# Kernel optimization log

Hardware: AMD Instinct MI355X
Metric: run time of the kernel (lower is better)

## Reference

```python
import jax, jax.numpy as jnp
import numpy as np

N_KERNELS = 5
MUL_FACTOR = 2.0


def setup_inputs() -> dict:
    key = jax.random.key(0)
    k1, k2 = jax.random.split(key)
    X = jax.random.normal(k1, (4096, 512), dtype=jnp.float32)
    Y = jax.random.normal(k2, (4096, 512), dtype=jnp.float32)
    return {"X": X, "Y": Y}


def _mmd(X, Y):
    # multipliers: 2.0 ** (arange(5) - 2) = [0.25, 0.5, 1, 2, 4]
    mults = MUL_FACTOR ** (jnp.arange(N_KERNELS, dtype=jnp.float32) - N_KERNELS // 2)
    Z = jnp.concatenate([X, Y], axis=0)            # [N+M, D]
    n = Z.shape[0]
    # squared euclidean pairwise distances (cdist ** 2)
    sq = jnp.sum(Z * Z, axis=-1)                    # [N+M]
    D2 = sq[:, None] + sq[None, :] - 2.0 * (Z @ Z.T)
    D2 = jnp.maximum(D2, 0.0)                       # [N+M, N+M]
    # bandwidth from detached distances: sum / (n^2 - n)
    bw = jax.lax.stop_gradient(jnp.sum(D2)) / (n * n - n)
    # multi-bandwidth RBF sum over kernels
    K = jnp.sum(jnp.exp(-D2[None, :, :] / (bw * mults)[:, None, None]), axis=0)
    Nx = X.shape[0]
    XX = jnp.mean(K[:Nx, :Nx])
    XY = jnp.mean(K[:Nx, Nx:])
    YY = jnp.mean(K[Nx:, Nx:])
    return XX - 2.0 * XY + YY


def reference(X, Y):
    return _mmd(X, Y)
```

## Files before the change

kernel.cpp:

```cpp
#include <hip/hip_runtime.h>

#define N_ROWS 8192
#define NX     4096
#define DIM    512
#define BT     128
#define NT     64
#define NTRI   2080
#define BK     32

typedef __bf16 bf16_t;
typedef bf16_t bf16x8 __attribute__((ext_vector_type(8)));
typedef float  f32x4  __attribute__((ext_vector_type(4)));

#if __has_builtin(__builtin_amdgcn_exp2f)
  #define EXP2F __builtin_amdgcn_exp2f
#else
  #define EXP2F exp2f
#endif


__device__ __forceinline__ const float* zrow(const float* X, const float* Y, int r) {
    return (r < NX) ? (X + (size_t)r * DIM) : (Y + (size_t)(r - NX) * DIM);
}

__device__ __forceinline__ void gload_lds16(const bf16_t* g, bf16_t* l) {
    __builtin_amdgcn_global_load_lds(
        (__attribute__((address_space(1))) void*)(void*)(g),
        (__attribute__((address_space(3))) void*)(void*)(l), 16, 0, 0);
}

__global__ void k_prep(const float* __restrict__ X, const float* __restrict__ Y,
                       bf16_t* __restrict__ Zh, float* __restrict__ sqrow,
                       float* __restrict__ colsum, unsigned* __restrict__ tk1,
                       double* __restrict__ S1acc) {
    int t = threadIdx.x;
    if (blockIdx.x == 0) {
        colsum[t] = 0.f; colsum[t + 256] = 0.f;
        if (t == 0) { *tk1 = 0u; *S1acc = 0.0; }
    }
    int wv = t >> 6, lane = t & 63;
    int row = blockIdx.x * 4 + wv;
    const float4* z4 = (const float4*)zrow(X, Y, row);
    float4 a = z4[lane * 2], b = z4[lane * 2 + 1];
    bf16x8 h;
    h[0] = (bf16_t)a.x; h[1] = (bf16_t)a.y; h[2] = (bf16_t)a.z; h[3] = (bf16_t)a.w;
    h[4] = (bf16_t)b.x; h[5] = (bf16_t)b.y; h[6] = (bf16_t)b.z; h[7] = (bf16_t)b.w;
    *(bf16x8*)(Zh + (size_t)row * DIM + lane * 8) = h;
    float s = a.x*a.x + a.y*a.y + a.z*a.z + a.w*a.w
            + b.x*b.x + b.y*b.y + b.z*b.z + b.w*b.w;
    #pragma unroll
    for (int off = 32; off > 0; off >>= 1) s += __shfl_down(s, off);
    if (lane == 0) sqrow[row] = s;
}

__global__ __launch_bounds__(512) void k_colsum(const bf16_t* __restrict__ Zh,
                                                const float* __restrict__ sqrow,
                                                float* __restrict__ colsum,
                                                float* __restrict__ cvals,
                                                double* __restrict__ S1acc,
                                                unsigned* __restrict__ tk1,
                                                double* __restrict__ acc,
                                                unsigned* __restrict__ tk2) {
    __shared__ float red[8][4][8];
    __shared__ double dred[512];
    __shared__ int is_last;
    int t = threadIdx.x, lane = t & 63, wv = t >> 6;
    int n16 = lane & 15, q16 = lane >> 4;
    int g = blockIdx.x & 15, slab = blockIdx.x >> 4;
    int c0 = g * 32 + q16 * 8;
    float s[8] = {0.f, 0.f, 0.f, 0.f, 0.f, 0.f, 0.f, 0.f};
    #pragma unroll
    for (int it = 0; it < 8; ++it) {
        int r = slab * 1024 + it * 128 + wv * 16 + n16;
        bf16x8 v = *(const bf16x8*)(Zh + (size_t)r * DIM + c0);
        #pragma unroll
        for (int j = 0; j < 8; ++j) s[j] += (float)v[j];
    }
    #pragma unroll
    for (int off = 8; off >= 1; off >>= 1)
        #pragma unroll
        for (int j = 0; j < 8; ++j) s[j] += __shfl_down(s[j], off);
    if (n16 == 0)
        #pragma unroll
        for (int j = 0; j < 8; ++j) red[wv][q16][j] = s[j];
    __syncthreads();
    float oldc = 0.f;
    if (t < 32) {
        int q = t >> 3, j = t & 7;
        float v = 0.f;
        #pragma unroll
        for (int w = 0; w < 8; ++w) v += red[w][q][j];
        oldc = atomicAdd(&colsum[g * 32 + q * 8 + j], v);
    }
    double olds = 0.0;
    if (g == 0) {
        int i = slab * 1024 + t;
        double d = (double)sqrow[i] + (double)sqrow[i + 512];
        #pragma unroll
        for (int off = 32; off > 0; off >>= 1) d += __shfl_down(d, off);
        if (lane == 0) olds = atomicAdd(S1acc, d);
    }
    asm volatile("" :: "v"(oldc), "v"(olds));
    asm volatile("s_waitcnt vmcnt(0)" ::: "memory");
    __syncthreads();
    if (t == 0) is_last = (atomicAdd(tk1, 1u) == 127u);
    __syncthreads();
    if (!is_last) return;
    float cv = atomicAdd(&colsum[t], 0.f);
    dred[t] = (double)cv * (double)cv;
    __syncthreads();
    for (int off = 256; off > 0; off >>= 1) {
        if (t < off) dred[t] += dred[t + off];
        __syncthreads();
    }
    if (t < 8) acc[t * 16] = 0.0;
    if (t == 0) {
        double S1 = atomicAdd(S1acc, 0.0);
        double n = (double)N_ROWS;
        double sumD2 = 2.0 * n * S1 - 2.0 * dred[0];
        double bw = sumD2 / (n * n - n);
        const double LOG2E = 1.4426950408889634;
        double mult = 0.25;
        for (int k = 0; k < 5; ++k) {
            cvals[k] = (float)(-LOG2E / (bw * mult));
            mult *= 2.0;
        }
        *tk2 = 0u;
    }
}

__global__ __launch_bounds__(256, 3) void k_pair(const bf16_t* __restrict__ Zh,
                                                 const float* __restrict__ sqrow,
                                                 const float* __restrict__ cvals,
                                                 double* __restrict__ acc,
                                                 unsigned* __restrict__ tk2,
                                                 float* __restrict__ out) {
    int L0 = blockIdx.x;
    int q = (L0 & 7) * (NTRI / 8) + (L0 >> 3);
    int ti, tj;
    {
        int I = 0, rem = q;
        #pragma unroll
        for (int it = 0; it < 8; ++it) {
            int rowcnt = 36 + (7 - I) * 64;
            if (rem >= rowcnt && I < 7) { rem -= rowcnt; ++I; } else break;
        }
        if (rem < 36) {
            int a = 0;
            #pragma unroll
            for (int it = 0; it < 7; ++it) {
                int nxt = (a + 1) * 8 - (a + 1) * a / 2;
                if (nxt <= rem) ++a; else break;
            }
            int off = a * 8 - a * (a - 1) / 2;
            ti = I * 8 + a;
            tj = I * 8 + a + (rem - off);
        } else {
            int r2 = rem - 36;
            int J = I + 1 + (r2 >> 6);
            int w = r2 & 63;
            ti = I * 8 + (w >> 3);
            tj = J * 8 + (w & 7);
        }
    }

    __shared__ bf16_t As[3][4096];
    __shared__ bf16_t Bs[3][4096];
    __shared__ float wsum[4];

    int t = threadIdx.x, lane = t & 63, wv = t >> 6;
    int wr = wv >> 1, wc = wv & 1;
    int i0 = ti * BT + wr * 64;
    int j0 = tj * BT + wc * 64;

    const bf16_t* gA[2]; const bf16_t* gB[2];
    {
        int c0 = t, r0 = c0 >> 2, sq0 = c0 & 3, q0 = sq0 ^ ((r0 >> 1) & 3);
        int c1 = 256 + t, r1 = c1 >> 2, sq1 = c1 & 3, q1 = sq1 ^ ((r1 >> 1) & 3);
        gA[0] = Zh + (size_t)(ti * BT + r0) * DIM + q0 * 8;
        gB[0] = Zh + (size_t)(tj * BT + r0) * DIM + q0 * 8;
        gA[1] = Zh + (size_t)(ti * BT + r1) * DIM + q1 * 8;
        gB[1] = Zh + (size_t)(tj * BT + r1) * DIM + q1 * 8;
    }
    int ldsoff0 = (wv * 64) * 8;
    int ldsoff1 = (256 + wv * 64) * 8;

    int n16 = lane & 15, q16 = lane >> 4;
    int aoff[4], boff[4];
    #pragma unroll
    for (int aa = 0; aa < 4; ++aa) {
        int r = 16 * (wr * 4 + aa) + n16;
        aoff[aa] = (r * 4 + (q16 ^ ((r >> 1) & 3))) * 8;
    }
    #pragma unroll
    for (int bb = 0; bb < 4; ++bb) {
        int r = 16 * (wc * 4 + bb) + n16;
        boff[bb] = (r * 4 + (q16 ^ ((r >> 1) & 3))) * 8;
    }

    float c4 = cvals[4];
    float sqi[4][4], sqj[4];
    #pragma unroll
    for (int aa = 0; aa < 4; ++aa)
        #pragma unroll
        for (int r = 0; r < 4; ++r)
            sqi[aa][r] = sqrow[i0 + 16 * aa + q16 * 4 + r];
    #pragma unroll
    for (int bb = 0; bb < 4; ++bb)
        sqj[bb] = sqrow[j0 + 16 * bb + n16];

    f32x4 accf[4][4];
    #pragma unroll
    for (int a = 0; a < 4; ++a)
        #pragma unroll
        for (int b = 0; b < 4; ++b)
            accf[a][b] = (f32x4){0.f, 0.f, 0.f, 0.f};

#define STAGE(S) do {                                   \
        int _b = (S) % 3; int _kn = (S) * BK;           \
        gload_lds16(gA[0] + _kn, &As[_b][ldsoff0]);     \
        gload_lds16(gB[0] + _kn, &Bs[_b][ldsoff0]);     \
        gload_lds16(gA[1] + _kn, &As[_b][ldsoff1]);     \
        gload_lds16(gB[1] + _kn, &Bs[_b][ldsoff1]);     \
    } while (0)

#define KSTEP(S, VM, DO_STAGE) do {                                          \
        asm volatile("s_waitcnt vmcnt(" VM ")" ::: "memory");                \
        __builtin_amdgcn_s_barrier();                                        \
        __builtin_amdgcn_sched_barrier(0);                                   \
        if (DO_STAGE) STAGE((S) + 2);                                        \
        const bf16_t* Ab = &As[(S) % 3][0];                                  \
        const bf16_t* Bb = &Bs[(S) % 3][0];                                  \
        bf16x8 a[4], b[4];                                                   \
        _Pragma("unroll")                                                    \
        for (int aa = 0; aa < 4; ++aa) a[aa] = *(const bf16x8*)(Ab + aoff[aa]); \
        _Pragma("unroll")                                                    \
        for (int bb = 0; bb < 4; ++bb) b[bb] = *(const bf16x8*)(Bb + boff[bb]); \
        __builtin_amdgcn_s_setprio(1);                                       \
        _Pragma("unroll")                                                    \
        for (int aa = 0; aa < 4; ++aa)                                       \
            _Pragma("unroll")                                                \
            for (int bb = 0; bb < 4; ++bb)                                   \
                accf[aa][bb] = __builtin_amdgcn_mfma_f32_16x16x32_bf16(      \
                    a[aa], b[bb], accf[aa][bb], 0, 0, 0);                    \
        __builtin_amdgcn_s_setprio(0);                                       \
    } while (0)

    STAGE(0); STAGE(1);
    KSTEP( 0, "4", 1); KSTEP( 1, "4", 1); KSTEP( 2, "4", 1); KSTEP( 3, "4", 1);
    KSTEP( 4, "4", 1); KSTEP( 5, "4", 1); KSTEP( 6, "4", 1); KSTEP( 7, "4", 1);
    KSTEP( 8, "4", 1); KSTEP( 9, "4", 1); KSTEP(10, "4", 1); KSTEP(11, "4", 1);
    KSTEP(12, "4", 1); KSTEP(13, "4", 1);
    KSTEP(14, "4", 0);
    KSTEP(15, "0", 0);
#undef KSTEP
#undef STAGE

    float s_local = 0.f;
    #pragma unroll
    for (int aa = 0; aa < 4; ++aa) {
        #pragma unroll
        for (int bb = 0; bb < 4; ++bb) {
            #pragma unroll
            for (int r = 0; r < 4; ++r) {
                float d2 = fmaf(-2.f, accf[aa][bb][r], sqi[aa][r] + sqj[bb]);
                d2 = fmaxf(d2, 0.f);
                float e4 = EXP2F(d2 * c4);
                float e3 = e4 * e4;
                float e2 = e3 * e3;
                float e1 = e2 * e2;
                float e0 = e1 * e1;
                s_local += e4 + e3 + e2 + e1 + e0;
            }
        }
    }
    #pragma unroll
    for (int off = 32; off > 0; off >>= 1) s_local += __shfl_down(s_local, off);
    if (lane == 0) wsum[wv] = s_local;
    __syncthreads();
    if (t == 0) {
        float bs = wsum[0] + wsum[1] + wsum[2] + wsum[3];
        double si = (ti < NT / 2) ? 1.0 : -1.0;
        double sj = (tj < NT / 2) ? 1.0 : -1.0;
        double w = si * sj * ((ti == tj) ? 1.0 : 2.0);
        double oldv = atomicAdd(&acc[(L0 & 7) * 16], w * (double)bs);
        asm volatile("" :: "v"(oldv));
        asm volatile("s_waitcnt vmcnt(0)" ::: "memory");
        unsigned old = atomicAdd(tk2, 1u);
        if (old == NTRI - 1) {
            double ssum = 0.0;
            #pragma unroll
            for (int i = 0; i < 8; ++i) ssum += atomicAdd(&acc[i * 16], 0.0);
            out[0] = (float)(ssum / ((double)NX * (double)NX));
        }
    }
}

extern "C" void kernel_launch(void* const* d_in, const int* in_sizes, int n_in,
                              void* d_out, int out_size, void* d_ws, size_t ws_size,
                              hipStream_t stream) {
    const float* X = (const float*)d_in[0];
    const float* Y = (const float*)d_in[1];
    float* out = (float*)d_out;

    float*    sqrow  = (float*)d_ws;
    float*    colsum = sqrow + 8192;
    float*    cvals  = (float*)((char*)d_ws + 34816);
    unsigned* tk1    = (unsigned*)((char*)d_ws + 34840);
    unsigned* tk2    = (unsigned*)((char*)d_ws + 34844);
    double*   S1acc  = (double*)((char*)d_ws + 34848);
    double*   acc    = (double*)((char*)d_ws + 34944);
    bf16_t*   Zh     = (bf16_t*)((char*)d_ws + 36864);

    k_prep  <<<2048, 256, 0, stream>>>(X, Y, Zh, sqrow, colsum, tk1, S1acc);
    k_colsum<<<128, 512, 0, stream>>>(Zh, sqrow, colsum, cvals, S1acc, tk1, acc, tk2);
    k_pair  <<<NTRI, 256, 0, stream>>>(Zh, sqrow, cvals, acc, tk2, out);
}
```

Before: 130.5 us.

## Make pair kernel persistent with cross-tile prefetch of next tile's stages

Launches 768 persistent blocks that each process two or three upper-triangle tile pairs instead of one block per tile. The first two K-stages of the next tile are prefetched during the last MFMA steps of the current tile, so the pipeline stays full across tiles. This targets block launch overhead, prologue latency and the tail of 2080 blocks spread over the CUs. It adds per-tile barriers, an atomic per tile, and a static split where some blocks get three tiles and others two, which can leave the load uneven.

```diff
diff --git a/kernel.cpp b/kernel.cpp
--- a/kernel.cpp
+++ b/kernel.cpp
@@ -7,6 +7,7 @@
 #define NT     64
 #define NTRI   2080
 #define BK     32
+#define NPERS  768
 
 typedef __bf16 bf16_t;
 typedef bf16_t bf16x8 __attribute__((ext_vector_type(8)));
@@ -135,33 +136,40 @@
                                                  double* __restrict__ acc,
                                                  unsigned* __restrict__ tk2,
                                                  float* __restrict__ out) {
-    int L0 = blockIdx.x;
-    int q = (L0 & 7) * (NTRI / 8) + (L0 >> 3);
-    int ti, tj;
-    {
-        int I = 0, rem = q;
-        #pragma unroll
-        for (int it = 0; it < 8; ++it) {
-            int rowcnt = 36 + (7 - I) * 64;
-            if (rem >= rowcnt && I < 7) { rem -= rowcnt; ++I; } else break;
-        }
-        if (rem < 36) {
-            int a = 0;
-            #pragma unroll
-            for (int it = 0; it < 7; ++it) {
-                int nxt = (a + 1) * 8 - (a + 1) * a / 2;
-                if (nxt <= rem) ++a; else break;
+    int b = blockIdx.x;
+    int ntile = (b < NTRI - 2 * NPERS) ? 3 : 2;
+    int tis[3], tjs[3];
+    #pragma unroll
+    for (int g = 0; g < 3; ++g) {
+        int T = b + g * NPERS;
+        int ti_ = 0, tj_ = 0;
+        if (T < NTRI) {
+            int q = (T & 7) * (NTRI / 8) + (T >> 3);
+            int I = 0, rem = q;
+            #pragma unroll
+            for (int it = 0; it < 8; ++it) {
+                int rowcnt = 36 + (7 - I) * 64;
+                if (rem >= rowcnt && I < 7) { rem -= rowcnt; ++I; } else break;
             }
-            int off = a * 8 - a * (a - 1) / 2;
-            ti = I * 8 + a;
-            tj = I * 8 + a + (rem - off);
-        } else {
-            int r2 = rem - 36;
-            int J = I + 1 + (r2 >> 6);
-            int w = r2 & 63;
-            ti = I * 8 + (w >> 3);
-            tj = J * 8 + (w & 7);
-        }
+            if (rem < 36) {
+                int a = 0;
+                #pragma unroll
+                for (int it = 0; it < 7; ++it) {
+                    int nxt = (a + 1) * 8 - (a + 1) * a / 2;
+                    if (nxt <= rem) ++a; else break;
+                }
+                int off = a * 8 - a * (a - 1) / 2;
+                ti_ = I * 8 + a;
+                tj_ = I * 8 + a + (rem - off);
+            } else {
+                int r2 = rem - 36;
+                int J = I + 1 + (r2 >> 6);
+                int w = r2 & 63;
+                ti_ = I * 8 + (w >> 3);
+                tj_ = J * 8 + (w & 7);
+            }
+        }
+        tis[g] = ti_; tjs[g] = tj_;
     }
 
     __shared__ bf16_t As[3][4096];
@@ -170,22 +178,14 @@
 
     int t = threadIdx.x, lane = t & 63, wv = t >> 6;
     int wr = wv >> 1, wc = wv & 1;
-    int i0 = ti * BT + wr * 64;
-    int j0 = tj * BT + wc * 64;
-
-    const bf16_t* gA[2]; const bf16_t* gB[2];
-    {
-        int c0 = t, r0 = c0 >> 2, sq0 = c0 & 3, q0 = sq0 ^ ((r0 >> 1) & 3);
-        int c1 = 256 + t, r1 = c1 >> 2, sq1 = c1 & 3, q1 = sq1 ^ ((r1 >> 1) & 3);
-        gA[0] = Zh + (size_t)(ti * BT + r0) * DIM + q0 * 8;
-        gB[0] = Zh + (size_t)(tj * BT + r0) * DIM + q0 * 8;
-        gA[1] = Zh + (size_t)(ti * BT + r1) * DIM + q1 * 8;
-        gB[1] = Zh + (size_t)(tj * BT + r1) * DIM + q1 * 8;
-    }
+    int n16 = lane & 15, q16 = lane >> 4;
+
+    int r0_, q0_, r1_, q1_;
+    { int c0 = t;       r0_ = c0 >> 2; q0_ = (c0 & 3) ^ ((r0_ >> 1) & 3);
+      int c1 = 256 + t; r1_ = c1 >> 2; q1_ = (c1 & 3) ^ ((r1_ >> 1) & 3); }
     int ldsoff0 = (wv * 64) * 8;
     int ldsoff1 = (256 + wv * 64) * 8;
 
-    int n16 = lane & 15, q16 = lane >> 4;
     int aoff[4], boff[4];
     #pragma unroll
     for (int aa = 0; aa < 4; ++aa) {
@@ -199,101 +199,145 @@
     }
 
     float c4 = cvals[4];
-    float sqi[4][4], sqj[4];
-    #pragma unroll
-    for (int aa = 0; aa < 4; ++aa)
-        #pragma unroll
-        for (int r = 0; r < 4; ++r)
-            sqi[aa][r] = sqrow[i0 + 16 * aa + q16 * 4 + r];
-    #pragma unroll
-    for (int bb = 0; bb < 4; ++bb)
-        sqj[bb] = sqrow[j0 + 16 * bb + n16];
-
-    f32x4 accf[4][4];
-    #pragma unroll
-    for (int a = 0; a < 4; ++a)
-        #pragma unroll
-        for (int b = 0; b < 4; ++b)
-            accf[a][b] = (f32x4){0.f, 0.f, 0.f, 0.f};
-
-#define STAGE(S) do {                                   \
-        int _b = (S) % 3; int _kn = (S) * BK;           \
-        gload_lds16(gA[0] + _kn, &As[_b][ldsoff0]);     \
-        gload_lds16(gB[0] + _kn, &Bs[_b][ldsoff0]);     \
-        gload_lds16(gA[1] + _kn, &As[_b][ldsoff1]);     \
-        gload_lds16(gB[1] + _kn, &Bs[_b][ldsoff1]);     \
+
+#define SETPTRS(TI, TJ, A0, B0, A1, B1) do {                        \
+        (A0) = Zh + (size_t)((TI) * BT + r0_) * DIM + q0_ * 8;      \
+        (B0) = Zh + (size_t)((TJ) * BT + r0_) * DIM + q0_ * 8;      \
+        (A1) = Zh + (size_t)((TI) * BT + r1_) * DIM + q1_ * 8;      \
+        (B1) = Zh + (size_t)((TJ) * BT + r1_) * DIM + q1_ * 8;      \
     } while (0)
 
-#define KSTEP(S, VM, DO_STAGE) do {                                          \
-        asm volatile("s_waitcnt vmcnt(" VM ")" ::: "memory");                \
-        __builtin_amdgcn_s_barrier();                                        \
-        __builtin_amdgcn_sched_barrier(0);                                   \
-        if (DO_STAGE) STAGE((S) + 2);                                        \
-        const bf16_t* Ab = &As[(S) % 3][0];                                  \
-        const bf16_t* Bb = &Bs[(S) % 3][0];                                  \
-        bf16x8 a[4], b[4];                                                   \
-        _Pragma("unroll")                                                    \
-        for (int aa = 0; aa < 4; ++aa) a[aa] = *(const bf16x8*)(Ab + aoff[aa]); \
-        _Pragma("unroll")                                                    \
-        for (int bb = 0; bb < 4; ++bb) b[bb] = *(const bf16x8*)(Bb + boff[bb]); \
-        __builtin_amdgcn_s_setprio(1);                                       \
-        _Pragma("unroll")                                                    \
-        for (int aa = 0; aa < 4; ++aa)                                       \
-            _Pragma("unroll")                                                \
-            for (int bb = 0; bb < 4; ++bb)                                   \
-                accf[aa][bb] = __builtin_amdgcn_mfma_f32_16x16x32_bf16(      \
-                    a[aa], b[bb], accf[aa][bb], 0, 0, 0);                    \
-        __builtin_amdgcn_s_setprio(0);                                       \
+#define STAGEP(A0, B0, A1, B1, KN, BUF) do {                        \
+        gload_lds16((A0) + (KN), &As[BUF][ldsoff0]);                \
+        gload_lds16((B0) + (KN), &Bs[BUF][ldsoff0]);                \
+        gload_lds16((A1) + (KN), &As[BUF][ldsoff1]);                \
+        gload_lds16((B1) + (KN), &Bs[BUF][ldsoff1]);                \
     } while (0)
 
-    STAGE(0); STAGE(1);
-    KSTEP( 0, "4", 1); KSTEP( 1, "4", 1); KSTEP( 2, "4", 1); KSTEP( 3, "4", 1);
-    KSTEP( 4, "4", 1); KSTEP( 5, "4", 1); KSTEP( 6, "4", 1); KSTEP( 7, "4", 1);
-    KSTEP( 8, "4", 1); KSTEP( 9, "4", 1); KSTEP(10, "4", 1); KSTEP(11, "4", 1);
-    KSTEP(12, "4", 1); KSTEP(13, "4", 1);
-    KSTEP(14, "4", 0);
-    KSTEP(15, "0", 0);
-#undef KSTEP
-#undef STAGE
-
-    float s_local = 0.f;
-    #pragma unroll
-    for (int aa = 0; aa < 4; ++aa) {
-        #pragma unroll
-        for (int bb = 0; bb < 4; ++bb) {
-            #pragma unroll
-            for (int r = 0; r < 4; ++r) {
-                float d2 = fmaf(-2.f, accf[aa][bb][r], sqi[aa][r] + sqj[bb]);
-                d2 = fmaxf(d2, 0.f);
-                float e4 = EXP2F(d2 * c4);
-                float e3 = e4 * e4;
-                float e2 = e3 * e3;
-                float e1 = e2 * e2;
-                float e0 = e1 * e1;
-                s_local += e4 + e3 + e2 + e1 + e0;
+#define WAITBAR(VM) do {                                            \
+        asm volatile("s_waitcnt vmcnt(" VM ")" ::: "memory");       \
+        __builtin_amdgcn_s_barrier();                               \
+        __builtin_amdgcn_sched_barrier(0);                          \
+    } while (0)
+
+#define DOMFMA(RB) do {                                             \
+        const bf16_t* Ab = &As[RB][0];                              \
+        const bf16_t* Bb = &Bs[RB][0];                              \
+        bf16x8 av[4], bv[4];                                        \
+        _Pragma("unroll")                                           \
+        for (int aa = 0; aa < 4; ++aa) av[aa] = *(const bf16x8*)(Ab + aoff[aa]); \
+        _Pragma("unroll")                                           \
+        for (int bb = 0; bb < 4; ++bb) bv[bb] = *(const bf16x8*)(Bb + boff[bb]); \
+        __builtin_amdgcn_s_setprio(1);                              \
+        _Pragma("unroll")                                           \
+        for (int aa = 0; aa < 4; ++aa)                              \
+            _Pragma("unroll")                                       \
+            for (int bb = 0; bb < 4; ++bb)                          \
+                accf[aa][bb] = __builtin_amdgcn_mfma_f32_16x16x32_bf16( \
+                    av[aa], bv[bb], accf[aa][bb], 0, 0, 0);         \
+        __builtin_amdgcn_s_setprio(0);                              \
+    } while (0)
+
+    const bf16_t *cA0, *cB0, *cA1, *cB1;
+    SETPTRS(tis[0], tjs[0], cA0, cB0, cA1, cB1);
+    STAGEP(cA0, cB0, cA1, cB1, 0, 0);
+    STAGEP(cA0, cB0, cA1, cB1, BK, 1);
+
+    #pragma unroll
+    for (int g = 0; g < 3; ++g) {
+        if (g >= ntile) break;
+        int has_next = (g + 1 < ntile);
+        const bf16_t *nA0 = cA0, *nB0 = cB0, *nA1 = cA1, *nB1 = cB1;
+        if (has_next) SETPTRS(tis[g + 1], tjs[g + 1], nA0, nB0, nA1, nB1);
+
+        f32x4 accf[4][4];
+        #pragma unroll
+        for (int a = 0; a < 4; ++a)
+            #pragma unroll
+            for (int bb = 0; bb < 4; ++bb)
+                accf[a][bb] = (f32x4){0.f, 0.f, 0.f, 0.f};
+
+        int rb = g % 3;
+        const bf16_t *pA0 = cA0 + 2 * BK, *pB0 = cB0 + 2 * BK;
+        const bf16_t *pA1 = cA1 + 2 * BK, *pB1 = cB1 + 2 * BK;
+        for (int s = 0; s < 14; ++s) {
+            WAITBAR("4");
+            int wb = rb + 2; if (wb >= 3) wb -= 3;
+            STAGEP(pA0, pB0, pA1, pB1, 0, wb);
+            pA0 += BK; pB0 += BK; pA1 += BK; pB1 += BK;
+            DOMFMA(rb);
+            ++rb; if (rb == 3) rb = 0;
+        }
+        WAITBAR("4");
+        if (has_next) STAGEP(nA0, nB0, nA1, nB1, 0, (g + 1) % 3);
+        DOMFMA((g + 2) % 3);
+        if (has_next) {
+            WAITBAR("4");
+            STAGEP(nA0, nB0, nA1, nB1, BK, (g + 2) % 3);
+        } else {
+            WAITBAR("0");
+        }
+        DOMFMA(g % 3);
+
+        int i0 = tis[g] * BT + wr * 64;
+        int j0 = tjs[g] * BT + wc * 64;
+        float sqi[4][4], sqj[4];
+        #pragma unroll
+        for (int aa = 0; aa < 4; ++aa)
+            #pragma unroll
+            for (int r = 0; r < 4; ++r)
+                sqi[aa][r] = sqrow[i0 + 16 * aa + q16 * 4 + r];
+        #pragma unroll
+        for (int bb = 0; bb < 4; ++bb)
+            sqj[bb] = sqrow[j0 + 16 * bb + n16];
+
+        float s_local = 0.f;
+        #pragma unroll
+        for (int aa = 0; aa < 4; ++aa) {
+            #pragma unroll
+            for (int bb = 0; bb < 4; ++bb) {
+                #pragma unroll
+                for (int r = 0; r < 4; ++r) {
+                    float d2 = fmaf(-2.f, accf[aa][bb][r], sqi[aa][r] + sqj[bb]);
+                    d2 = fmaxf(d2, 0.f);
+                    float e4 = EXP2F(d2 * c4);
+                    float e3 = e4 * e4;
+                    float e2 = e3 * e3;
+                    float e1 = e2 * e2;
+                    float e0 = e1 * e1;
+                    s_local += e4 + e3 + e2 + e1 + e0;
+                }
             }
         }
-    }
-    #pragma unroll
-    for (int off = 32; off > 0; off >>= 1) s_local += __shfl_down(s_local, off);
-    if (lane == 0) wsum[wv] = s_local;
-    __syncthreads();
+        #pragma unroll
+        for (int off = 32; off > 0; off >>= 1) s_local += __shfl_down(s_local, off);
+        if (lane == 0) wsum[wv] = s_local;
+        __syncthreads();
+        if (t == 0) {
+            float bs = wsum[0] + wsum[1] + wsum[2] + wsum[3];
+            double si = (tis[g] < NT / 2) ? 1.0 : -1.0;
+            double sj = (tjs[g] < NT / 2) ? 1.0 : -1.0;
+            double w = si * sj * ((tis[g] == tjs[g]) ? 1.0 : 2.0);
+            double oldv = atomicAdd(&acc[(b & 7) * 16], w * (double)bs);
+            asm volatile("" :: "v"(oldv));
+        }
+        if (has_next) { cA0 = nA0; cB0 = nB0; cA1 = nA1; cB1 = nB1; }
+    }
+
     if (t == 0) {
-        float bs = wsum[0] + wsum[1] + wsum[2] + wsum[3];
-        double si = (ti < NT / 2) ? 1.0 : -1.0;
-        double sj = (tj < NT / 2) ? 1.0 : -1.0;
-        double w = si * sj * ((ti == tj) ? 1.0 : 2.0);
-        double oldv = atomicAdd(&acc[(L0 & 7) * 16], w * (double)bs);
-        asm volatile("" :: "v"(oldv));
         asm volatile("s_waitcnt vmcnt(0)" ::: "memory");
         unsigned old = atomicAdd(tk2, 1u);
-        if (old == NTRI - 1) {
+        if (old == NPERS - 1) {
             double ssum = 0.0;
             #pragma unroll
             for (int i = 0; i < 8; ++i) ssum += atomicAdd(&acc[i * 16], 0.0);
             out[0] = (float)(ssum / ((double)NX * (double)NX));
         }
     }
+#undef SETPTRS
+#undef STAGEP
+#undef WAITBAR
+#undef DOMFMA
 }
 
 extern "C" void kernel_launch(void* const* d_in, const int* in_sizes, int n_in,
@@ -314,5 +358,5 @@
 
     k_prep  <<<2048, 256, 0, stream>>>(X, Y, Zh, sqrow, colsum, tk1, S1acc);
     k_colsum<<<128, 512, 0, stream>>>(Zh, sqrow, colsum, cvals, S1acc, tk1, acc, tk2);
-    k_pair  <<<NTRI, 256, 0, stream>>>(Zh, sqrow, cvals, acc, tk2, out);
-}
+    k_pair  <<<NPERS, 256, 0, stream>>>(Zh, sqrow, cvals, acc, tk2, out);
+}
```

Result: no change. 132.2 us (+1.3%).

## Merge column-sum reduction into prep kernel reading fp32 inputs directly

Applied to the files above, without the earlier changes.

The separate column-sum kernel is folded into the prep launch as 128 extra blocks. Those blocks read the fp32 X/Y directly and compute the column sums and the squared-norm total themselves, so they no longer depend on the bf16 copy or on sqrow. A tiny zeroing kernel is added in front to reset the counters. This is meant to remove one dependent launch boundary and run the bandwidth statistics concurrently with the bf16 conversion, at the cost of re-reading the fp32 inputs and adding one small kernel. The bandwidth statistic now comes from unrounded fp32 values rather than bf16-rounded ones.

```diff
diff --git a/kernel.cpp b/kernel.cpp
--- a/kernel.cpp
+++ b/kernel.cpp
@@ -7,6 +7,8 @@
 #define NT     64
 #define NTRI   2080
 #define BK     32
+#define NMAIN  2048
+#define NCS    128
 
 typedef __bf16 bf16_t;
 typedef bf16_t bf16x8 __attribute__((ext_vector_type(8)));
@@ -29,103 +31,98 @@
         (__attribute__((address_space(3))) void*)(void*)(l), 16, 0, 0);
 }
 
+__global__ void k_zero(float* __restrict__ colsum, unsigned* __restrict__ tk1,
+                       double* __restrict__ S1acc) {
+    int t = threadIdx.x;
+    colsum[t] = 0.f; colsum[t + 256] = 0.f;
+    if (t == 0) { *tk1 = 0u; *S1acc = 0.0; }
+}
+
 __global__ void k_prep(const float* __restrict__ X, const float* __restrict__ Y,
                        bf16_t* __restrict__ Zh, float* __restrict__ sqrow,
-                       float* __restrict__ colsum, unsigned* __restrict__ tk1,
-                       double* __restrict__ S1acc) {
-    int t = threadIdx.x;
-    if (blockIdx.x == 0) {
-        colsum[t] = 0.f; colsum[t + 256] = 0.f;
-        if (t == 0) { *tk1 = 0u; *S1acc = 0.0; }
-    }
-    int wv = t >> 6, lane = t & 63;
-    int row = blockIdx.x * 4 + wv;
-    const float4* z4 = (const float4*)zrow(X, Y, row);
-    float4 a = z4[lane * 2], b = z4[lane * 2 + 1];
-    bf16x8 h;
-    h[0] = (bf16_t)a.x; h[1] = (bf16_t)a.y; h[2] = (bf16_t)a.z; h[3] = (bf16_t)a.w;
-    h[4] = (bf16_t)b.x; h[5] = (bf16_t)b.y; h[6] = (bf16_t)b.z; h[7] = (bf16_t)b.w;
-    *(bf16x8*)(Zh + (size_t)row * DIM + lane * 8) = h;
-    float s = a.x*a.x + a.y*a.y + a.z*a.z + a.w*a.w
-            + b.x*b.x + b.y*b.y + b.z*b.z + b.w*b.w;
-    #pragma unroll
-    for (int off = 32; off > 0; off >>= 1) s += __shfl_down(s, off);
-    if (lane == 0) sqrow[row] = s;
-}
-
-__global__ __launch_bounds__(512) void k_colsum(const bf16_t* __restrict__ Zh,
-                                                const float* __restrict__ sqrow,
-                                                float* __restrict__ colsum,
-                                                float* __restrict__ cvals,
-                                                double* __restrict__ S1acc,
-                                                unsigned* __restrict__ tk1,
-                                                double* __restrict__ acc,
-                                                unsigned* __restrict__ tk2) {
-    __shared__ float red[8][4][8];
-    __shared__ double dred[512];
-    __shared__ int is_last;
+                       float* __restrict__ colsum, float* __restrict__ cvals,
+                       unsigned* __restrict__ tk1, unsigned* __restrict__ tk2,
+                       double* __restrict__ S1acc, double* __restrict__ acc) {
+    __shared__ float  redc[32][8][4];
+    __shared__ double redd[4];
+    __shared__ double dred2[256];
+    __shared__ int    is_last;
+    int bid = blockIdx.x;
     int t = threadIdx.x, lane = t & 63, wv = t >> 6;
-    int n16 = lane & 15, q16 = lane >> 4;
-    int g = blockIdx.x & 15, slab = blockIdx.x >> 4;
-    int c0 = g * 32 + q16 * 8;
-    float s[8] = {0.f, 0.f, 0.f, 0.f, 0.f, 0.f, 0.f, 0.f};
-    #pragma unroll
-    for (int it = 0; it < 8; ++it) {
-        int r = slab * 1024 + it * 128 + wv * 16 + n16;
-        bf16x8 v = *(const bf16x8*)(Zh + (size_t)r * DIM + c0);
-        #pragma unroll
-        for (int j = 0; j < 8; ++j) s[j] += (float)v[j];
-    }
-    #pragma unroll
-    for (int off = 8; off >= 1; off >>= 1)
-        #pragma unroll
-        for (int j = 0; j < 8; ++j) s[j] += __shfl_down(s[j], off);
-    if (n16 == 0)
-        #pragma unroll
-        for (int j = 0; j < 8; ++j) red[wv][q16][j] = s[j];
-    __syncthreads();
-    float oldc = 0.f;
+
+    if (bid < NMAIN) {
+        if (bid == 0) {
+            if (t < 8) acc[t * 16] = 0.0;
+            if (t == 0) *tk2 = 0u;
+        }
+        int row = bid * 4 + wv;
+        const float4* z4 = (const float4*)zrow(X, Y, row);
+        float4 a = z4[lane * 2], b = z4[lane * 2 + 1];
+        bf16x8 h;
+        h[0] = (bf16_t)a.x; h[1] = (bf16_t)a.y; h[2] = (bf16_t)a.z; h[3] = (bf16_t)a.w;
+        h[4] = (bf16_t)b.x; h[5] = (bf16_t)b.y; h[6] = (bf16_t)b.z; h[7] = (bf16_t)b.w;
+        *(bf16x8*)(Zh + (size_t)row * DIM + lane * 8) = h;
+        float s = a.x*a.x + a.y*a.y + a.z*a.z + a.w*a.w
+                + b.x*b.x + b.y*b.y + b.z*b.z + b.w*b.w;
+        #pragma unroll
+        for (int off = 32; off > 0; off >>= 1) s += __shfl_down(s, off);
+        if (lane == 0) sqrow[row] = s;
+        return;
+    }
+
+    int cb = bid - NMAIN;
+    int g = cb & 15, slab = cb >> 4;
+    const float* base = (slab < 4) ? (X + (size_t)slab * 1024 * DIM)
+                                   : (Y + (size_t)(slab - 4) * 1024 * DIM);
+    int c4off = g * 32 + (t & 7) * 4;
+    int rl0 = t >> 3;
+    float cs0 = 0.f, cs1 = 0.f, cs2 = 0.f, cs3 = 0.f;
+    double ssq = 0.0;
+    for (int it = 0; it < 32; ++it) {
+        float4 v = *(const float4*)(base + (size_t)(it * 32 + rl0) * DIM + c4off);
+        cs0 += v.x; cs1 += v.y; cs2 += v.z; cs3 += v.w;
+        ssq += (double)v.x * v.x + (double)v.y * v.y
+             + (double)v.z * v.z + (double)v.w * v.w;
+    }
+    redc[rl0][t & 7][0] = cs0; redc[rl0][t & 7][1] = cs1;
+    redc[rl0][t & 7][2] = cs2; redc[rl0][t & 7][3] = cs3;
+    #pragma unroll
+    for (int off = 32; off > 0; off >>= 1) ssq += __shfl_down(ssq, off);
+    if (lane == 0) redd[wv] = ssq;
+    __syncthreads();
+    float oldc = 0.f; double olds = 0.0;
     if (t < 32) {
-        int q = t >> 3, j = t & 7;
         float v = 0.f;
         #pragma unroll
-        for (int w = 0; w < 8; ++w) v += red[w][q][j];
-        oldc = atomicAdd(&colsum[g * 32 + q * 8 + j], v);
-    }
-    double olds = 0.0;
-    if (g == 0) {
-        int i = slab * 1024 + t;
-        double d = (double)sqrow[i] + (double)sqrow[i + 512];
-        #pragma unroll
-        for (int off = 32; off > 0; off >>= 1) d += __shfl_down(d, off);
-        if (lane == 0) olds = atomicAdd(S1acc, d);
-    }
+        for (int r = 0; r < 32; ++r) v += redc[r][t >> 2][t & 3];
+        oldc = atomicAdd(&colsum[g * 32 + t], v);
+    }
+    if (t == 0)
+        olds = atomicAdd(S1acc, redd[0] + redd[1] + redd[2] + redd[3]);
     asm volatile("" :: "v"(oldc), "v"(olds));
     asm volatile("s_waitcnt vmcnt(0)" ::: "memory");
     __syncthreads();
-    if (t == 0) is_last = (atomicAdd(tk1, 1u) == 127u);
+    if (t == 0) is_last = (atomicAdd(tk1, 1u) == NCS - 1u);
     __syncthreads();
     if (!is_last) return;
-    float cv = atomicAdd(&colsum[t], 0.f);
-    dred[t] = (double)cv * (double)cv;
-    __syncthreads();
-    for (int off = 256; off > 0; off >>= 1) {
-        if (t < off) dred[t] += dred[t + off];
+    float cv0 = atomicAdd(&colsum[t], 0.f);
+    float cv1 = atomicAdd(&colsum[t + 256], 0.f);
+    dred2[t] = (double)cv0 * cv0 + (double)cv1 * cv1;
+    __syncthreads();
+    for (int off = 128; off > 0; off >>= 1) {
+        if (t < off) dred2[t] += dred2[t + off];
         __syncthreads();
     }
-    if (t < 8) acc[t * 16] = 0.0;
     if (t == 0) {
         double S1 = atomicAdd(S1acc, 0.0);
         double n = (double)N_ROWS;
-        double sumD2 = 2.0 * n * S1 - 2.0 * dred[0];
-        double bw = sumD2 / (n * n - n);
+        double bw = (2.0 * n * S1 - 2.0 * dred2[0]) / (n * n - n);
         const double LOG2E = 1.4426950408889634;
         double mult = 0.25;
         for (int k = 0; k < 5; ++k) {
             cvals[k] = (float)(-LOG2E / (bw * mult));
             mult *= 2.0;
         }
-        *tk2 = 0u;
     }
 }
 
@@ -312,7 +309,8 @@
     double*   acc    = (double*)((char*)d_ws + 34944);
     bf16_t*   Zh     = (bf16_t*)((char*)d_ws + 36864);
 
-    k_prep  <<<2048, 256, 0, stream>>>(X, Y, Zh, sqrow, colsum, tk1, S1acc);
-    k_colsum<<<128, 512, 0, stream>>>(Zh, sqrow, colsum, cvals, S1acc, tk1, acc, tk2);
-    k_pair  <<<NTRI, 256, 0, stream>>>(Zh, sqrow, cvals, acc, tk2, out);
-}
+    k_zero<<<1, 256, 0, stream>>>(colsum, tk1, S1acc);
+    k_prep<<<NMAIN + NCS, 256, 0, stream>>>(X, Y, Zh, sqrow, colsum, cvals,
+                                            tk1, tk2, S1acc, acc);
+    k_pair<<<NTRI, 256, 0, stream>>>(Zh, sqrow, cvals, acc, tk2, out);
+}
```

After: 132.2 us. About the same (+1.3%).
